# Kernel tuning notes

Hardware: AMD Instinct MI355X
Metric: run time of the kernel (lower is better)

Reference implementation:

```python
import jax, jax.numpy as jnp
import numpy as np

H, D, EF, NT, ET = 4, 32, 32, 4, 8
N, E = 100000, 1600000
NEG_SLOPE = 0.2


def setup_inputs() -> dict:
    key = jax.random.key(0)
    ks = jax.random.split(key, 11)
    return {
        "feat": jax.random.normal(ks[0], (N, H * D), jnp.float32),
        "fc": jax.random.normal(ks[1], (NT, H, D), jnp.float32) * 0.1,
        "edge_emb": jax.random.normal(ks[2], (ET, EF), jnp.float32),
        "W_e": jax.random.normal(ks[3], (H * EF, EF), jnp.float32) * 0.1,
        "attn_l": jax.random.normal(ks[4], (1, H, D), jnp.float32) * 0.1,
        "attn_r": jax.random.normal(ks[5], (1, H, D), jnp.float32) * 0.1,
        "attn_e": jax.random.normal(ks[6], (1, H, EF), jnp.float32) * 0.1,
        "node_types": jax.random.randint(ks[7], (N,), 0, NT, jnp.int32),
        "e_feat": jax.random.randint(ks[8], (E,), 0, ET, jnp.int32),
        "src": jax.random.randint(ks[9], (E,), 0, N, jnp.int32),
        "dst": jax.random.randint(ks[10], (E,), 0, N, jnp.int32),
    }


def reference(feat, fc, edge_emb, W_e, attn_l, attn_r, attn_e, node_types, e_feat, src, dst):
    n = feat.shape[0]
    h = feat.reshape(n, H, D)                      # [N,H,D] (h_src == h_dst)
    fs = h * fc[node_types]                        # per-node-type scaling, feat_src == feat_dst

    # edge-type embedding path: Embedding -> Linear(edge_feats, H*edge_feats) -> attn_e score
    emb = (edge_emb @ W_e.T).reshape(ET, H, EF)    # [ET,H,EF]
    ee = (emb * attn_e).sum(-1)[e_feat]            # [E,H]

    el = (fs * attn_l).sum(-1)                     # [N,H]
    er = (fs * attn_r).sum(-1)                     # [N,H]
    e = jax.nn.leaky_relu(el[src] + er[dst] + ee, NEG_SLOPE)  # [E,H]

    # edge_softmax: segment softmax over destination node
    m = jax.ops.segment_max(e, dst, num_segments=n)           # [N,H]
    ex = jnp.exp(e - m[dst])
    s = jax.ops.segment_sum(ex, dst, num_segments=n)          # [N,H]
    a = ex / s[dst]                                            # [E,H]

    # u_mul_e + sum aggregation
    msg = fs[src] * a[:, :, None]                              # [E,H,D]
    rst = jax.ops.segment_sum(msg, dst, num_segments=n)       # [N,H,D]

    rst = rst + h                                              # residual (Identity, in==out feats)
    return rst, a[:, :, None]
```

## Files before the change

kernel.cpp:

```cpp
#include <hip/hip_runtime.h>
#include <stdint.h>

namespace {
constexpr int kH = 4, kD = 32, kEF = 32, kNT = 4, kET = 8;
constexpr int kHD = kH * kD;
constexpr float kNegSlope = 0.2f;
constexpr int kBN = 128;
constexpr int kNB = (100000 + kBN - 1) / kBN;
constexpr int kHB = 512;
constexpr int kXP = 20;

using f32x2 = __attribute__((ext_vector_type(2))) float;
using f32x4 = __attribute__((ext_vector_type(4))) float;

__device__ __forceinline__ float lrelu(float x) { return x > 0.f ? x : kNegSlope * x; }

__global__ void __launch_bounds__(256) k_init(
    const float* __restrict__ feat, const float* __restrict__ fc,
    const float* __restrict__ edge_emb, const float* __restrict__ W_e,
    const float* __restrict__ attn_l, const float* __restrict__ attn_r,
    const float* __restrict__ attn_e, const int* __restrict__ node_types,
    const int* __restrict__ dst, int* __restrict__ partial,
    float* __restrict__ el, float* __restrict__ ernv, uint8_t* __restrict__ fs,
    float* __restrict__ ee_tab, int N, int E) {
  __shared__ int hh[kNB];
  if (blockIdx.x < kHB) {
    for (int i = threadIdx.x; i < kNB; i += 256) hh[i] = 0;
    __syncthreads();
    int per = (E + kHB - 1) / kHB;
    int e0 = blockIdx.x * per;
    int e1 = min(e0 + per, E);
    for (int i = e0 + threadIdx.x; i < e1; i += 256) atomicAdd(&hh[dst[i] >> 7], 1);
    __syncthreads();
    for (int i = threadIdx.x; i < kNB; i += 256) partial[blockIdx.x * kNB + i] = hh[i];
  }
  if (blockIdx.x == 0 && threadIdx.x < kET * kH) {
    int et = threadIdx.x / kH, h = threadIdx.x % kH;
    float acc = 0.f;
    for (int f = 0; f < kEF; ++f) {
      const float* wrow = W_e + (h * kEF + f) * kEF;
      const float* erow = edge_emb + et * kEF;
      float emb = 0.f;
      for (int k = 0; k < kEF; ++k) emb += erow[k] * wrow[k];
      acc += emb * attn_e[h * kEF + f];
    }
    ee_tab[et * kH + h] = acc;
  }
  int gid = blockIdx.x * blockDim.x + threadIdx.x;
  int node = gid >> 5;
  int lane = threadIdx.x & 31;
  if (node >= N) return;
  int nt = node_types[node];
  float4 f4 = *(const float4*)(feat + (size_t)(node << 7) + lane * 4);
  float4 c4 = *(const float4*)(fc + nt * kHD + lane * 4);
  float4 al = *(const float4*)(attn_l + lane * 4);
  float4 ar = *(const float4*)(attn_r + lane * 4);
  float fx = f4.x * c4.x, fy = f4.y * c4.y, fz = f4.z * c4.z, fw = f4.w * c4.w;
  int w = __builtin_amdgcn_cvt_pk_fp8_f32(fx, fy, 0, false);
  w = __builtin_amdgcn_cvt_pk_fp8_f32(fz, fw, w, true);
  *(int*)(fs + (size_t)(node << 7) + lane * 4) = w;
  float pl = fx * al.x + fy * al.y + fz * al.z + fw * al.w;
  float pr = fx * ar.x + fy * ar.y + fz * ar.z + fw * ar.w;
#pragma unroll
  for (int off = 1; off < 8; off <<= 1) {
    pl += __shfl_xor(pl, off);
    pr += __shfl_xor(pr, off);
  }
  if ((lane & 7) == 0) {
    int h = lane >> 3;
    el[node * kH + h] = pl;
    ernv[(node << 3) + h] = pr;
  }
}

__global__ void __launch_bounds__(256) k_scanA(int* __restrict__ partial,
                                               int* __restrict__ btot) {
  __shared__ int bufa[kHB], bufb[kHB];
  int b = blockIdx.x, t = threadIdx.x;
  bufa[t] = partial[t * kNB + b];
  bufa[t + 256] = partial[(t + 256) * kNB + b];
  __syncthreads();
  int* cur = bufa;
  int* nxt = bufb;
  for (int off = 1; off < kHB; off <<= 1) {
    for (int i = t; i < kHB; i += 256) nxt[i] = cur[i] + (i >= off ? cur[i - off] : 0);
    __syncthreads();
    int* sw = cur; cur = nxt; nxt = sw;
  }
  partial[t * kNB + b] = t ? cur[t - 1] : 0;
  partial[(t + 256) * kNB + b] = cur[t + 255];
  if (t == 0) btot[b] = cur[kHB - 1];
}

__global__ void __launch_bounds__(256) k_scatter2(
    const int* __restrict__ dst, const int* __restrict__ src,
    const int* __restrict__ e_feat, const int* __restrict__ partial,
    const int* __restrict__ btot, int* __restrict__ tmp, int E) {
  __shared__ int h[kNB], sA[kNB], sB[kNB], bb[kNB];
  int t = threadIdx.x;
  for (int i = t; i < kNB; i += 256) sA[i] = btot[i];
  __syncthreads();
  int* cur = sA;
  int* nxt = sB;
  for (int off = 1; off < kNB; off <<= 1) {
    for (int i = t; i < kNB; i += 256) nxt[i] = cur[i] + (i >= off ? cur[i - off] : 0);
    __syncthreads();
    int* sw = cur; cur = nxt; nxt = sw;
  }
  for (int i = t; i < kNB; i += 256) {
    bb[i] = i ? cur[i - 1] : 0;
    h[i] = 0;
  }
  __syncthreads();
  int per = (E + gridDim.x - 1) / gridDim.x;
  int e0 = blockIdx.x * per;
  int e1 = min(e0 + per, E);
  const int* myrow = partial + blockIdx.x * kNB;
  for (int i = e0 + t; i < e1; i += 256) {
    int d = dst[i];
    int b = d >> 7;
    int lr = atomicAdd(&h[b], 1);
    int pos = bb[b] + myrow[b] + lr;
    tmp[pos] = src[i] | (e_feat[i] << 17) | ((d & 127) << 20);
  }
}

__global__ void __launch_bounds__(256) k_build(const int* __restrict__ btot,
                                               const int* __restrict__ tmp,
                                               int* __restrict__ ptr,
                                               int* __restrict__ csr, int N, int E) {
  __shared__ int fh[128], fb[128], sc[128];
  __shared__ int red[256];
  int b = blockIdx.x, t = threadIdx.x;
  int acc = 0;
  for (int i = t; i < b; i += 256) acc += btot[i];
  red[t] = acc;
  __syncthreads();
  for (int off = 128; off > 0; off >>= 1) {
    if (t < off) red[t] += red[t + off];
    __syncthreads();
  }
  int s0 = red[0];
  int s1 = s0 + btot[b];
  if (t < 128) fh[t] = 0;
  __syncthreads();
  for (int j = s0 + t; j < s1; j += 256) atomicAdd(&fh[tmp[j] >> 20], 1);
  __syncthreads();
  if (t < 128) sc[t] = fh[t];
  __syncthreads();
  for (int off = 1; off < 128; off <<= 1) {
    int v = 0;
    if (t < 128 && t >= off) v = sc[t - off];
    __syncthreads();
    if (t < 128) sc[t] += v;
    __syncthreads();
  }
  if (t < 128) {
    fb[t] = sc[t] - fh[t];
    int d = (b << 7) + t;
    if (d < N) ptr[d] = s0 + fb[t];
    fh[t] = 0;
  }
  if (b == gridDim.x - 1 && t == 0) ptr[N] = E;
  __syncthreads();
  for (int j = s0 + t; j < s1; j += 256) {
    int v = tmp[j];
    int dl = v >> 20;
    int r = atomicAdd(&fh[dl], 1);
    csr[s0 + fb[dl] + r] = v & 0xFFFFF;
  }
}

__global__ void __launch_bounds__(256) k_fused(
    const uint8_t* __restrict__ fs, const float* __restrict__ feat,
    const float* __restrict__ el, float* __restrict__ ernv,
    const float* __restrict__ ee_tab, const int* __restrict__ ptr,
    const int* __restrict__ csr, float* __restrict__ rst, int N) {
  __shared__ float ee_sh[kET * kH];
  __shared__ __align__(16) float xp[4][64 * kXP];
  if (threadIdx.x < kET * kH) ee_sh[threadIdx.x] = ee_tab[threadIdx.x];
  __syncthreads();
  int lane = threadIdx.x & 63;
  int wid = threadIdx.x >> 6;
  int node = blockIdx.x * 4 + wid;
  if (node >= N) return;
  int start = ptr[node], end = ptr[node + 1];

  int g = lane >> 3;
  int q = lane & 7;
  int head = q >> 1;
  int qoff = q << 4;
  float er_h = ernv[(node << 3) + head];
  f32x2 f2 = *(const f32x2*)(feat + ((size_t)node << 7) + lane * 2);

  float sm = 0.f;
  f32x2 acc[8];
#pragma unroll
  for (int k = 0; k < 8; ++k) acc[k] = (f32x2){0.f, 0.f};

  int j = start + g;
  int pk0 = csr[(j < end) ? j : 0];
  int pk1 = csr[(j + 8 < end) ? j + 8 : 0];
  int s0 = pk0 & 0x1FFFF;
  float elv0 = el[(s0 << 2) + head];
  int4 w0 = *(const int4*)(fs + ((size_t)s0 << 7) + qoff);
  float ee0 = ee_sh[((pk0 >> 17) << 2) + head];
  int s1 = pk1 & 0x1FFFF;
  float elv1 = el[(s1 << 2) + head];
  int4 w1 = *(const int4*)(fs + ((size_t)s1 << 7) + qoff);
  float ee1 = ee_sh[((pk1 >> 17) << 2) + head];
  int pk2 = csr[(j + 16 < end) ? j + 16 : 0];

  while (j < end) {
    int s2 = pk2 & 0x1FFFF;
    float elv2 = el[(s2 << 2) + head];
    int4 w2 = *(const int4*)(fs + ((size_t)s2 << 7) + qoff);
    float ee2 = ee_sh[((pk2 >> 17) << 2) + head];
    int pk3 = csr[(j + 24 < end) ? j + 24 : 0];
    float ex = __expf(lrelu(elv0 + er_h + ee0));
    sm += ex;
    f32x2 ex2 = {ex, ex};
#pragma unroll
    for (int c = 0; c < 4; ++c) {
      int wc = c == 0 ? w0.x : c == 1 ? w0.y : c == 2 ? w0.z : w0.w;
      acc[2 * c + 0] += ex2 * __builtin_amdgcn_cvt_pk_f32_fp8(wc, false);
      acc[2 * c + 1] += ex2 * __builtin_amdgcn_cvt_pk_f32_fp8(wc, true);
    }
    elv0 = elv1; w0 = w1; ee0 = ee1;
    elv1 = elv2; w1 = w2; ee1 = ee2;
    pk2 = pk3;
    j += 8;
  }

  sm += __shfl_xor(sm, 8);
  sm += __shfl_xor(sm, 16);
  sm += __shfl_xor(sm, 32);
  float rinv = sm > 0.f ? 1.f / sm : 0.f;

  float* row = &xp[wid][lane * kXP];
#pragma unroll
  for (int c = 0; c < 4; ++c) {
    float4 v4 = {acc[2 * c].x, acc[2 * c].y, acc[2 * c + 1].x, acc[2 * c + 1].y};
    *(float4*)(row + c * 4) = v4;
  }
  asm volatile("s_waitcnt lgkmcnt(0)" ::: "memory");
  __builtin_amdgcn_sched_barrier(0);
  int qsrc = lane >> 3;
  int coff = (lane & 7) * 2;
  const float* base = &xp[wid][qsrc * kXP + coff];
  f32x2 v = {0.f, 0.f};
#pragma unroll
  for (int gg = 0; gg < 8; ++gg) v += *(const f32x2*)(base + gg * 8 * kXP);

  float rs = __shfl(rinv, (lane >> 4) << 1);
  float rb = __shfl(rinv, lane << 1);
  f32x2 o = v * rs + f2;
  __builtin_nontemporal_store(o, (f32x2*)(rst + ((size_t)node << 7) + lane * 2));
  if (lane < kH) ernv[(node << 3) + 4 + lane] = rb;
}

__global__ void __launch_bounds__(256) k_post(
    const int* __restrict__ src, const int* __restrict__ dst,
    const int* __restrict__ e_feat, const float* __restrict__ el,
    const float* __restrict__ ernv, const float* __restrict__ ee_tab,
    float* __restrict__ out_a, int E) {
  int i = blockIdx.x * blockDim.x + threadIdx.x;
  if (i >= E) return;
  int s = src[i], d = dst[i], et = e_feat[i];
  float4 elv = *(const float4*)(el + s * kH);
  float4 erv = *(const float4*)(ernv + ((size_t)d << 3));
  float4 rv = *(const float4*)(ernv + ((size_t)d << 3) + 4);
  float4 ee = *(const float4*)(ee_tab + et * kH);
  f32x4 a;
  a.x = __expf(lrelu(elv.x + erv.x + ee.x)) * rv.x;
  a.y = __expf(lrelu(elv.y + erv.y + ee.y)) * rv.y;
  a.z = __expf(lrelu(elv.z + erv.z + ee.z)) * rv.z;
  a.w = __expf(lrelu(elv.w + erv.w + ee.w)) * rv.w;
  __builtin_nontemporal_store(a, (f32x4*)(out_a + (size_t)i * kH));
}

}

extern "C" void kernel_launch(void* const* d_in, const int* in_sizes, int n_in,
                              void* d_out, int out_size, void* d_ws, size_t ws_size,
                              hipStream_t stream) {
  const float* feat = (const float*)d_in[0];
  const float* fc = (const float*)d_in[1];
  const float* edge_emb = (const float*)d_in[2];
  const float* W_e = (const float*)d_in[3];
  const float* attn_l = (const float*)d_in[4];
  const float* attn_r = (const float*)d_in[5];
  const float* attn_e = (const float*)d_in[6];
  const int* node_types = (const int*)d_in[7];
  const int* e_feat = (const int*)d_in[8];
  const int* src = (const int*)d_in[9];
  const int* dst = (const int*)d_in[10];
  int N = in_sizes[7];
  int E = in_sizes[8];

  char* ws = (char*)d_ws;
  size_t off = 0;
  auto alloc = [&](size_t bytes) -> void* {
    void* p = ws + off;
    off = (off + bytes + 255) & ~(size_t)255;
    return p;
  };
  float* ee_tab = (float*)alloc((size_t)kET * kH * sizeof(float));
  float* el = (float*)alloc((size_t)N * kH * sizeof(float));
  float* ernv = (float*)alloc((size_t)N * 2 * kH * sizeof(float));
  uint8_t* fs = (uint8_t*)alloc((size_t)N * kHD * sizeof(uint8_t));
  int* partial = (int*)alloc((size_t)kHB * kNB * sizeof(int));
  int* btot = (int*)alloc((size_t)kNB * sizeof(int));
  int* ptr = (int*)alloc((size_t)(N + 1) * sizeof(int));
  int* tmp = (int*)alloc((size_t)E * sizeof(int));
  int* csr = (int*)alloc((size_t)E * sizeof(int));

  k_init<<<(N + 7) / 8, 256, 0, stream>>>(feat, fc, edge_emb, W_e, attn_l, attn_r,
                                          attn_e, node_types, dst, partial, el,
                                          ernv, fs, ee_tab, N, E);
  k_scanA<<<kNB, 256, 0, stream>>>(partial, btot);
  k_scatter2<<<kHB, 256, 0, stream>>>(dst, src, e_feat, partial, btot, tmp, E);
  k_build<<<kNB, 256, 0, stream>>>(btot, tmp, ptr, csr, N, E);

  float* rst = (float*)d_out;
  float* out_a = (float*)d_out + (size_t)N * kHD;
  k_fused<<<(N + 3) / 4, 256, 0, stream>>>(fs, feat, el, ernv, ee_tab, ptr, csr,
                                           rst, N);
  k_post<<<(E + 255) / 256, 256, 0, stream>>>(src, dst, e_feat, el, ernv, ee_tab,
                                              out_a, E);
}
```

Before: 296.0 us.

## Replace two-pass bucket counting sort with fixed-capacity slabs and global atomic cursors

Measured after the change: 292.6 us. About the same (-1.1%).

```diff
diff --git a/kernel.cpp b/kernel.cpp
--- a/kernel.cpp
+++ b/kernel.cpp
@@ -8,6 +8,7 @@
 constexpr int kBN = 128;
 constexpr int kNB = (100000 + kBN - 1) / kBN;
 constexpr int kHB = 512;
+constexpr int kCap = 4096;
 constexpr int kXP = 20;
 
 using f32x2 = __attribute__((ext_vector_type(2))) float;
@@ -20,31 +21,22 @@
     const float* __restrict__ edge_emb, const float* __restrict__ W_e,
     const float* __restrict__ attn_l, const float* __restrict__ attn_r,
     const float* __restrict__ attn_e, const int* __restrict__ node_types,
-    const int* __restrict__ dst, int* __restrict__ partial,
-    float* __restrict__ el, float* __restrict__ ernv, uint8_t* __restrict__ fs,
-    float* __restrict__ ee_tab, int N, int E) {
-  __shared__ int hh[kNB];
-  if (blockIdx.x < kHB) {
-    for (int i = threadIdx.x; i < kNB; i += 256) hh[i] = 0;
-    __syncthreads();
-    int per = (E + kHB - 1) / kHB;
-    int e0 = blockIdx.x * per;
-    int e1 = min(e0 + per, E);
-    for (int i = e0 + threadIdx.x; i < e1; i += 256) atomicAdd(&hh[dst[i] >> 7], 1);
-    __syncthreads();
-    for (int i = threadIdx.x; i < kNB; i += 256) partial[blockIdx.x * kNB + i] = hh[i];
-  }
-  if (blockIdx.x == 0 && threadIdx.x < kET * kH) {
-    int et = threadIdx.x / kH, h = threadIdx.x % kH;
-    float acc = 0.f;
-    for (int f = 0; f < kEF; ++f) {
-      const float* wrow = W_e + (h * kEF + f) * kEF;
-      const float* erow = edge_emb + et * kEF;
-      float emb = 0.f;
-      for (int k = 0; k < kEF; ++k) emb += erow[k] * wrow[k];
-      acc += emb * attn_e[h * kEF + f];
+    int* __restrict__ cursor, float* __restrict__ el, float* __restrict__ ernv,
+    uint8_t* __restrict__ fs, float* __restrict__ ee_tab, int N) {
+  if (blockIdx.x == 0) {
+    for (int i = threadIdx.x; i < kNB; i += 256) cursor[i] = 0;
+    if (threadIdx.x < kET * kH) {
+      int et = threadIdx.x / kH, h = threadIdx.x % kH;
+      float acc = 0.f;
+      for (int f = 0; f < kEF; ++f) {
+        const float* wrow = W_e + (h * kEF + f) * kEF;
+        const float* erow = edge_emb + et * kEF;
+        float emb = 0.f;
+        for (int k = 0; k < kEF; ++k) emb += erow[k] * wrow[k];
+        acc += emb * attn_e[h * kEF + f];
+      }
+      ee_tab[et * kH + h] = acc;
     }
-    ee_tab[et * kH + h] = acc;
   }
   int gid = blockIdx.x * blockDim.x + threadIdx.x;
   int node = gid >> 5;
@@ -73,59 +65,33 @@
   }
 }
 
-__global__ void __launch_bounds__(256) k_scanA(int* __restrict__ partial,
-                                               int* __restrict__ btot) {
-  __shared__ int bufa[kHB], bufb[kHB];
-  int b = blockIdx.x, t = threadIdx.x;
-  bufa[t] = partial[t * kNB + b];
-  bufa[t + 256] = partial[(t + 256) * kNB + b];
-  __syncthreads();
-  int* cur = bufa;
-  int* nxt = bufb;
-  for (int off = 1; off < kHB; off <<= 1) {
-    for (int i = t; i < kHB; i += 256) nxt[i] = cur[i] + (i >= off ? cur[i - off] : 0);
-    __syncthreads();
-    int* sw = cur; cur = nxt; nxt = sw;
-  }
-  partial[t * kNB + b] = t ? cur[t - 1] : 0;
-  partial[(t + 256) * kNB + b] = cur[t + 255];
-  if (t == 0) btot[b] = cur[kHB - 1];
-}
-
-__global__ void __launch_bounds__(256) k_scatter2(
+__global__ void __launch_bounds__(256) k_scatter3(
     const int* __restrict__ dst, const int* __restrict__ src,
-    const int* __restrict__ e_feat, const int* __restrict__ partial,
-    const int* __restrict__ btot, int* __restrict__ tmp, int E) {
-  __shared__ int h[kNB], sA[kNB], sB[kNB], bb[kNB];
+    const int* __restrict__ e_feat, int* __restrict__ cursor,
+    int* __restrict__ tmp, int E) {
+  __shared__ int h[kNB], r[kNB];
   int t = threadIdx.x;
-  for (int i = t; i < kNB; i += 256) sA[i] = btot[i];
-  __syncthreads();
-  int* cur = sA;
-  int* nxt = sB;
-  for (int off = 1; off < kNB; off <<= 1) {
-    for (int i = t; i < kNB; i += 256) nxt[i] = cur[i] + (i >= off ? cur[i - off] : 0);
-    __syncthreads();
-    int* sw = cur; cur = nxt; nxt = sw;
-  }
-  for (int i = t; i < kNB; i += 256) {
-    bb[i] = i ? cur[i - 1] : 0;
-    h[i] = 0;
-  }
+  for (int i = t; i < kNB; i += 256) h[i] = 0;
   __syncthreads();
   int per = (E + gridDim.x - 1) / gridDim.x;
   int e0 = blockIdx.x * per;
   int e1 = min(e0 + per, E);
-  const int* myrow = partial + blockIdx.x * kNB;
+  for (int i = e0 + t; i < e1; i += 256) atomicAdd(&h[dst[i] >> 7], 1);
+  __syncthreads();
+  for (int i = t; i < kNB; i += 256) {
+    int c = h[i];
+    r[i] = i * kCap + (c ? atomicAdd(&cursor[i], c) : 0);
+  }
+  __syncthreads();
   for (int i = e0 + t; i < e1; i += 256) {
     int d = dst[i];
     int b = d >> 7;
-    int lr = atomicAdd(&h[b], 1);
-    int pos = bb[b] + myrow[b] + lr;
+    int pos = atomicAdd(&r[b], 1);
     tmp[pos] = src[i] | (e_feat[i] << 17) | ((d & 127) << 20);
   }
 }
 
-__global__ void __launch_bounds__(256) k_build(const int* __restrict__ btot,
+__global__ void __launch_bounds__(256) k_build(const int* __restrict__ cursor,
                                                const int* __restrict__ tmp,
                                                int* __restrict__ ptr,
                                                int* __restrict__ csr, int N, int E) {
@@ -133,7 +99,7 @@
   __shared__ int red[256];
   int b = blockIdx.x, t = threadIdx.x;
   int acc = 0;
-  for (int i = t; i < b; i += 256) acc += btot[i];
+  for (int i = t; i < b; i += 256) acc += cursor[i];
   red[t] = acc;
   __syncthreads();
   for (int off = 128; off > 0; off >>= 1) {
@@ -141,10 +107,11 @@
     __syncthreads();
   }
   int s0 = red[0];
-  int s1 = s0 + btot[b];
+  int cnt = min(cursor[b], kCap);
+  const int* slab = tmp + (size_t)b * kCap;
   if (t < 128) fh[t] = 0;
   __syncthreads();
-  for (int j = s0 + t; j < s1; j += 256) atomicAdd(&fh[tmp[j] >> 20], 1);
+  for (int j = t; j < cnt; j += 256) atomicAdd(&fh[slab[j] >> 20], 1);
   __syncthreads();
   if (t < 128) sc[t] = fh[t];
   __syncthreads();
@@ -163,8 +130,8 @@
   }
   if (b == gridDim.x - 1 && t == 0) ptr[N] = E;
   __syncthreads();
-  for (int j = s0 + t; j < s1; j += 256) {
-    int v = tmp[j];
+  for (int j = t; j < cnt; j += 256) {
+    int v = slab[j];
     int dl = v >> 20;
     int r = atomicAdd(&fh[dl], 1);
     csr[s0 + fb[dl] + r] = v & 0xFFFFF;
@@ -309,18 +276,16 @@
   float* el = (float*)alloc((size_t)N * kH * sizeof(float));
   float* ernv = (float*)alloc((size_t)N * 2 * kH * sizeof(float));
   uint8_t* fs = (uint8_t*)alloc((size_t)N * kHD * sizeof(uint8_t));
-  int* partial = (int*)alloc((size_t)kHB * kNB * sizeof(int));
-  int* btot = (int*)alloc((size_t)kNB * sizeof(int));
+  int* cursor = (int*)alloc((size_t)kNB * sizeof(int));
   int* ptr = (int*)alloc((size_t)(N + 1) * sizeof(int));
-  int* tmp = (int*)alloc((size_t)E * sizeof(int));
+  int* tmp = (int*)alloc((size_t)kNB * kCap * sizeof(int));
   int* csr = (int*)alloc((size_t)E * sizeof(int));
 
   k_init<<<(N + 7) / 8, 256, 0, stream>>>(feat, fc, edge_emb, W_e, attn_l, attn_r,
-                                          attn_e, node_types, dst, partial, el,
-                                          ernv, fs, ee_tab, N, E);
-  k_scanA<<<kNB, 256, 0, stream>>>(partial, btot);
-  k_scatter2<<<kHB, 256, 0, stream>>>(dst, src, e_feat, partial, btot, tmp, E);
-  k_build<<<kNB, 256, 0, stream>>>(btot, tmp, ptr, csr, N, E);
+                                          attn_e, node_types, cursor, el, ernv, fs,
+                                          ee_tab, N);
+  k_scatter3<<<kHB, 256, 0, stream>>>(dst, src, e_feat, cursor, tmp, E);
+  k_build<<<kNB, 256, 0, stream>>>(cursor, tmp, ptr, csr, N, E);
 
   float* rst = (float*)d_out;
   float* out_a = (float*)d_out + (size_t)N * kHD;
```
